# Optimization experiments

Hardware: AMD Instinct MI355X
Metric: run time of the kernel (lower is better)

The kernel has to match this reference:

```python
import jax, jax.numpy as jnp
import numpy as np

N = 64
K_CHEB = 5
EPS = 1e-5

# db4 decomposition filters (scaling_filter.mat Lo_D / Hi_D, length 8)
_LO = np.array([-0.010597401784997278, 0.032883011666982945, 0.030841381835986965,
                -0.18703481171888114, -0.02798376941698385, 0.6308807679295904,
                0.7148465705525415, 0.23037781330885523], dtype=np.float32)
_HI = np.array([-0.23037781330885523, 0.7148465705525415, -0.6308807679295904,
                -0.02798376941698385, 0.18703481171888114, 0.030841381835986965,
                0.032883011666982945, -0.010597401784997278], dtype=np.float32)
# torch stores np.flip(filters) and Conv2d does cross-correlation -> use flipped taps here too
_KERN = np.stack([_LO[::-1], _HI[::-1]])[:, None, None, :].copy()  # [2,1,1,8]


def _wavelet_step(x):
    # x: [B, C, 1, W]; circular pad 3 each side, depthwise len-8 conv, stride 2
    p = 3  # filter_length // 2 - 1
    xp = jnp.concatenate([x[..., -p:], x, x[..., :p]], axis=-1)
    b, c, h, wp = xp.shape
    out = jax.lax.conv_general_dilated(
        xp.reshape(b * c, 1, h, wp), jnp.asarray(_KERN), (1, 2), 'VALID',
        dimension_numbers=('NCHW', 'OIHW', 'NCHW'))
    out = out.reshape(b, c, 2, h, -1)
    return out[:, :, 0], out[:, :, 1]  # (approx, detail)


def _cbam(x, fc1, fc2, sa_w):
    # x: [B, 657, 1, 64]; channel attention then spatial attention
    def mlp(v):  # v: [B, C, 1, 1]
        h = jax.nn.relu(jnp.einsum('oc,bchw->bohw', fc1, v))
        return jnp.einsum('oc,bchw->bohw', fc2, h)
    avg = x.mean(axis=(2, 3), keepdims=True)
    mx = x.max(axis=(2, 3), keepdims=True)
    x = x * jax.nn.sigmoid(mlp(avg) + mlp(mx))
    s = jnp.concatenate([x.mean(axis=1, keepdims=True), x.max(axis=1, keepdims=True)], axis=1)
    sa = jax.nn.sigmoid(jax.lax.conv_general_dilated(
        s, sa_w, (1, 1), ((3, 3), (3, 3)), dimension_numbers=('NCHW', 'OIHW', 'NCHW')))
    return x * sa


def _global_edge_weight(w_tril, mask):
    xs, ys = np.tril_indices(N)
    E = jnp.zeros((N, N), w_tril.dtype).at[xs, ys].set(w_tril)
    E = E + E.T - jnp.diag(jnp.diag(E))
    return (E * mask).reshape(-1)


def _norm_adj(edges, w):
    # PyG NewSGConv.norm: add remaining self-loops (fill=1), deg from |w|, sym normalize
    row, col = edges[0], edges[1]
    has_self = jnp.zeros((N,), w.dtype).at[row].add(jnp.where(row == col, 1.0, 0.0)) > 0
    w_self = jnp.where(has_self, 0.0, 1.0).astype(w.dtype)
    deg = jnp.zeros((N,), w.dtype).at[row].add(jnp.abs(w)) + w_self
    dsafe = jnp.where(deg > 0, deg, 1.0)
    dinv = jnp.where(deg > 0, jax.lax.rsqrt(dsafe), 0.0)
    norm = dinv[row] * w * dinv[col]
    A = jnp.zeros((N, N), w.dtype).at[col, row].add(norm)  # out[i] = sum_j A[i,j] x[j]
    return A + jnp.diag(dinv * w_self * dinv)


def _gcn_block(x, A, W, b, g, be):
    # x: [B, N, C_in]; K-hop SGConv propagation, linear, train-mode batchnorm over (B, N)
    for _ in range(K_CHEB):
        x = jnp.einsum('ij,bjc->bic', A, x)
    x = x @ W.T + b
    mean = x.mean(axis=(0, 1))
    var = x.var(axis=(0, 1))
    return (x - mean) * jax.lax.rsqrt(var + EPS) * g + be


def _classify(x, W1, b1, g, be, W2, b2):
    out = x.reshape(x.shape[0], -1) @ W1.T + b1
    out = (out - out.mean(0)) * jax.lax.rsqrt(out.var(0) + EPS) * g + be
    return jax.nn.log_softmax(out @ W2.T + b2, axis=1)


def _forward(x, local_graph_weight, global_mask, ca_fc1, ca_fc2, sa_conv, edge_weight_tril,
             ld_W, ld_b, ld_g, ld_be, ld1_W, ld1_b, ld1_g, ld1_be,
             d_W, d_b, d_g, d_be, d1_W, d1_b, d1_g, d1_be,
             cls_W1, cls_b1, cls_g, cls_be, cls_W2, cls_b2, edges):
    xc = jnp.transpose(x, (0, 3, 2, 1))        # [B, 657, 1, 64]
    xc = _cbam(xc, ca_fc1, ca_fc2, sa_conv)
    xh = jnp.transpose(xc, (0, 3, 2, 1))       # [B, 64, 1, 657]
    # fi = floor(log2(200)) = 7 -> 4 decomposition levels: 657->328->164->82->41
    out1, _gamma = _wavelet_step(xh)
    out2, _beta = _wavelet_step(out1)
    out3, _alpha = _wavelet_step(out2)
    delta, _theta = _wavelet_step(out3)        # [B, 64, 1, 41]
    delta = delta[:, :, 0, :]                  # squeeze -> [B, 64, 41]
    gw = _global_edge_weight(edge_weight_tril, global_mask)
    A_loc = _norm_adj(edges, local_graph_weight)
    A_glb = _norm_adj(edges, gw)
    lf = _gcn_block(delta, A_loc, ld_W, ld_b, ld_g, ld_be)
    lf = _gcn_block(lf, A_loc, ld1_W, ld1_b, ld1_g, ld1_be)
    gf = _gcn_block(delta, A_glb, d_W, d_b, d_g, d_be)
    gf = _gcn_block(gf, A_glb, d1_W, d1_b, d1_g, d1_be)
    feat = jnp.concatenate([lf.mean(-1, keepdims=True), gf.mean(-1, keepdims=True)], axis=2)  # [B,64,2]
    return _classify(feat, cls_W1, cls_b1, cls_g, cls_be, cls_W2, cls_b2)


def setup_inputs() -> dict:
    key = jax.random.key(0)
    ks = iter(jax.random.split(key, 16))
    B = 512
    f32 = jnp.float32
    def rn(shape, s=0.05):
        return jax.random.normal(next(ks), shape, f32) * s
    ii = jnp.arange(N, dtype=jnp.int32)
    edges = jnp.stack([jnp.repeat(ii, N), jnp.tile(ii, N)])  # full 64x64 mesh (incl. self loops)
    return dict(
        x=jax.random.normal(next(ks), (B, N, 1, 657), f32),
        local_graph_weight=jax.random.uniform(next(ks), (N * N,), f32),
        global_mask=jnp.ones((N, N), f32),
        ca_fc1=rn((82, 657)),
        ca_fc2=rn((657, 82)),
        sa_conv=rn((1, 2, 7, 7), 0.1),
        edge_weight_tril=jax.random.uniform(next(ks), (N * (N + 1) // 2,), f32),
        ld_W=rn((16, 41)), ld_b=jnp.zeros(16, f32), ld_g=jnp.ones(16, f32), ld_be=jnp.zeros(16, f32),
        ld1_W=rn((4, 16)), ld1_b=jnp.zeros(4, f32), ld1_g=jnp.ones(4, f32), ld1_be=jnp.zeros(4, f32),
        d_W=rn((16, 41)), d_b=jnp.zeros(16, f32), d_g=jnp.ones(16, f32), d_be=jnp.zeros(16, f32),
        d1_W=rn((4, 16)), d1_b=jnp.zeros(4, f32), d1_g=jnp.ones(4, f32), d1_be=jnp.zeros(4, f32),
        cls_W1=rn((32, 128)), cls_b1=jnp.zeros(32, f32), cls_g=jnp.ones(32, f32), cls_be=jnp.zeros(32, f32),
        cls_W2=rn((2, 32)), cls_b2=jnp.zeros(2, f32),
        edges=edges,
    )


def reference(x, local_graph_weight, global_mask, ca_fc1, ca_fc2, sa_conv, edge_weight_tril,
              ld_W, ld_b, ld_g, ld_be, ld1_W, ld1_b, ld1_g, ld1_be,
              d_W, d_b, d_g, d_be, d1_W, d1_b, d1_g, d1_be,
              cls_W1, cls_b1, cls_g, cls_be, cls_W2, cls_b2, edges):
    return _forward(x, local_graph_weight, global_mask, ca_fc1, ca_fc2, sa_conv, edge_weight_tril,
                    ld_W, ld_b, ld_g, ld_be, ld1_W, ld1_b, ld1_g, ld1_be,
                    d_W, d_b, d_g, d_be, d1_W, d1_b, d1_g, d1_be,
                    cls_W1, cls_b1, cls_g, cls_be, cls_W2, cls_b2, edges)
```

## Files before the change

kernel.cpp:

```cpp
#include <hip/hip_runtime.h>
#include <math.h>

#define NB 512
#define NN 64
#define TL 657
#define LV1 328
#define LV2 164
#define LV3 82
#define LV4 41
#define HID 82
#define ST 66

#define WS_M      0
#define WS_ACC    32768
#define WS_SMEAN  36864
#define WS_SMAX   167936
#define WS_CATT   3373568
#define WS_Y1     682496
#define WS_DELTA  4876800
#define WS_Y2     4876800
#define WS_OUT1   5925376

#define ACC_Y1 0
#define ACC_Y2 64
#define ACC_O1 80

__device__ __forceinline__ float sigmoidf_(float v){ return 1.0f/(1.0f+expf(-v)); }

__device__ __forceinline__ void wav_level(float* __restrict__ dst, const float* __restrict__ src,
                                          int outL, int inL, int lane){
  const float DLO[8] = {0.23037781330885523f, 0.7148465705525415f, 0.6308807679295904f,
                        -0.02798376941698385f, -0.18703481171888114f, 0.030841381835986965f,
                        0.032883011666982945f, -0.010597401784997278f};
  for (int k=lane; k<outL; k+=64){
    int i0 = 2*k - 3;
    float a = 0.f;
    #pragma unroll
    for (int j=0;j<8;j++){
      int idx = i0 + j;
      idx = (idx < 0) ? idx + inL : ((idx >= inL) ? idx - inL : idx);
      a += src[idx]*DLO[j];
    }
    dst[k] = a;
  }
}

__device__ __forceinline__ void mm16(float* __restrict__ D, int dstride,
                                     const float* __restrict__ A, const float* __restrict__ Bm){
  int tid = threadIdx.x;
  int wv = tid >> 6, lane = tid & 63;
  int i0 = wv*4;
  float a4[4] = {0.f,0.f,0.f,0.f};
  #pragma unroll
  for (int kc=0; kc<4; kc++){
    float bb[16];
    #pragma unroll
    for (int j=0;j<16;j++) bb[j] = Bm[(kc*16+j)*ST + lane];
    #pragma unroll
    for (int i=0;i<4;i++){
      const float2* ar = (const float2*)&A[(i0+i)*ST + kc*16];
      float s0=0.f, s1=0.f;
      #pragma unroll
      for (int j2=0;j2<8;j2++){
        float2 v = ar[j2];
        s0 += v.x*bb[2*j2]; s1 += v.y*bb[2*j2+1];
      }
      a4[i] += s0+s1;
    }
  }
  #pragma unroll
  for (int i=0;i<4;i++) D[(i0+i)*dstride + lane] = a4[i];
}

__global__ __launch_bounds__(1024) void k_front(
    const float* __restrict__ x,
    const float* __restrict__ lgw, const float* __restrict__ gmask,
    const float* __restrict__ tril, const int* __restrict__ edges,
    const float* __restrict__ fc1, const float* __restrict__ fc2,
    float* __restrict__ catt_g,
    float* __restrict__ Mout, double* __restrict__ acc)
{
  __shared__ float smem[3*NN*ST];
  __shared__ float deg[64], hs[64], dinv[64], wself[64];
  int tid = threadIdx.x;
  int bid = blockIdx.x;
  int wv = tid>>6, lane = tid&63;
  int b = bid;

  if (bid < 2){
    float* Wbuf = smem;
    float* Amat = smem + NN*ST;
    float* P1   = smem + 2*NN*ST;
    int g = bid;
    if (g==0 && tid<512) acc[tid]=0.0;
    for (int e=tid;e<4096;e+=1024){
      float w;
      if (g==0) w = lgw[e];
      else {
        int i=e>>6, j=e&63;
        int aa = (i>j)? i:j, bb = (i>j)? j:i;
        w = tril[aa*(aa+1)/2 + bb] * gmask[e];
      }
      Wbuf[e] = w;
    }
    for (int i=tid;i<NN*ST;i+=1024) Amat[i] = 0.f;
    if (tid<64){ deg[tid]=0.f; hs[tid]=0.f; }
    __syncthreads();
    {
      int e0 = tid*4;
      int runr = edges[e0];
      float runv = 0.f;
      #pragma unroll
      for (int i=0;i<4;i++){
        int e = e0+i;
        int r = edges[e];
        int c = edges[4096+e];
        float w = Wbuf[e];
        if (r != runr){ atomicAdd(&deg[runr], runv); runr = r; runv = 0.f; }
        runv += fabsf(w);
        if (r == c) hs[r] = 1.f;
      }
      atomicAdd(&deg[runr], runv);
    }
    __syncthreads();
    if (tid<64){
      float w_ = (hs[tid] > 0.f) ? 0.f : 1.f;
      float d = deg[tid] + w_;
      dinv[tid] = (d > 0.f) ? rsqrtf(d) : 0.f;
      wself[tid] = w_;
    }
    __syncthreads();
    for (int e=tid;e<4096;e+=1024){
      int r = edges[e], c = edges[4096+e];
      float nm = dinv[r]*Wbuf[e]*dinv[c];
      atomicAdd(&Amat[c*ST+r], nm);
    }
    __syncthreads();
    if (tid<64) Amat[tid*ST+tid] += dinv[tid]*wself[tid]*dinv[tid];
    __syncthreads();
    mm16(P1,   ST, Amat, Amat); __syncthreads();
    mm16(Wbuf, ST, P1,   P1);   __syncthreads();
    mm16(&Mout[g*4096], 64, Wbuf, Amat);
    __syncthreads();
  }

  {
    float s[11], m[11];
    #pragma unroll
    for (int i=0;i<11;i++){ s[i]=0.f; m[i]=-INFINITY; }
    const float* xb = x + (size_t)b*NN*TL;
    for (int r=0;r<4;r++){
      const float* row = xb + (size_t)(wv*4 + r)*TL;
      #pragma unroll
      for (int i=0;i<11;i++){
        int t = lane + 64*i;
        if (t < TL){
          float v = row[t];
          s[i] += v; m[i] = fmaxf(m[i], v);
        }
      }
    }
    for (int step=8; step>=1; step>>=1){
      if (wv >= step && wv < 2*step){
        float* bs = smem + (wv-step)*1328;
        #pragma unroll
        for (int i=0;i<11;i++){
          int t = lane + 64*i;
          if (t<TL){ bs[t] = s[i]; bs[664+t] = m[i]; }
        }
      }
      __syncthreads();
      if (wv < step){
        float* bs = smem + wv*1328;
        #pragma unroll
        for (int i=0;i<11;i++){
          int t = lane + 64*i;
          if (t<TL){ s[i] += bs[t]; m[i] = fmaxf(m[i], bs[664+t]); }
        }
      }
      __syncthreads();
    }
    float* cs = smem;
    float* cm = smem + 664;
    float* h  = smem + 1400;
    if (wv==0){
      #pragma unroll
      for (int i=0;i<11;i++){
        int t = lane + 64*i;
        if (t<TL){ cs[t] = s[i]; cm[t] = m[i]; }
      }
    }
    __syncthreads();
    for (int o=wv; o<HID; o+=16){
      const float* fr = fc1 + (size_t)o*TL;
      float a = 0.f, bm = 0.f;
      #pragma unroll
      for (int i=0;i<11;i++){
        int c = lane + 64*i;
        if (c < TL){
          float f = fr[c];
          a += f*cs[c]; bm += f*cm[c];
        }
      }
      #pragma unroll
      for (int off=32;off;off>>=1){
        a  += __shfl_xor(a,off);
        bm += __shfl_xor(bm,off);
      }
      if (lane==0)
        h[o] = fmaxf(a*(1.0f/64.0f),0.f) + fmaxf(bm,0.f);
    }
    __syncthreads();
    if (tid < TL){
      const float2* fr = (const float2*)(fc2 + (size_t)tid*HID);
      float a0=0.f, a1=0.f;
      #pragma unroll
      for (int u2=0;u2<41;u2++){
        float2 v = fr[u2];
        a0 += v.x*h[2*u2]; a1 += v.y*h[2*u2+1];
      }
      catt_g[(size_t)b*TL + tid] = sigmoidf_(a0+a1);
    }
  }
}

__global__ __launch_bounds__(256) void k_wav(
    const float* __restrict__ x, const float* __restrict__ catt_g,
    float* __restrict__ delta, float* __restrict__ smean, float* __restrict__ smax)
{
  __shared__ float catt[TL];
  __shared__ float yb[4][TL];
  __shared__ float o1b[4][LV1];
  __shared__ float o2b[4][LV2];
  __shared__ float o3b[4][LV3];
  int tid = threadIdx.x, b = blockIdx.x;
  for (int i=tid;i<TL;i+=256) catt[i] = catt_g[(size_t)b*TL + i];
  __syncthreads();
  int wv = tid>>6, lane = tid&63;
  int n = blockIdx.y*4 + wv;
  float* y  = yb[wv];
  float* p1 = o1b[wv];
  float* p2 = o2b[wv];
  float* p3 = o3b[wv];
  const float DLO[8] = {0.23037781330885523f, 0.7148465705525415f, 0.6308807679295904f,
                        -0.02798376941698385f, -0.18703481171888114f, 0.030841381835986965f,
                        0.032883011666982945f, -0.010597401784997278f};
  const float* row = x + ((size_t)b*NN + n)*TL;
  float ls = 0.f, lm = -INFINITY;
  #pragma unroll
  for (int i=0;i<11;i++){
    int t = lane + 64*i;
    if (t < TL){
      float v = row[t]*catt[t];
      y[t] = v; ls += v; lm = fmaxf(lm,v);
    }
  }
  #pragma unroll
  for (int off=32;off;off>>=1){
    ls += __shfl_xor(ls,off);
    lm = fmaxf(lm, __shfl_xor(lm,off));
  }
  if (lane==0){ smean[b*NN+n] = ls*(1.0f/657.0f); smax[b*NN+n] = lm; }
  wav_level(p1, y,  LV1, TL,  lane);
  wav_level(p2, p1, LV2, LV1, lane);
  wav_level(p3, p2, LV3, LV2, lane);
  if (lane < LV4){
    int i0 = 2*lane - 3;
    float a = 0.f;
    #pragma unroll
    for (int j=0;j<8;j++){
      int idx = i0 + j;
      idx = (idx < 0) ? idx + LV3 : ((idx >= LV3) ? idx - LV3 : idx);
      a += p3[idx]*DLO[j];
    }
    delta[((size_t)b*NN + n)*LV4 + lane] = a;
  }
}

__global__ __launch_bounds__(256) void k_gcn1(
  const float* __restrict__ delta, const float* __restrict__ Mmat,
  const float* __restrict__ smean, const float* __restrict__ smax,
  const float* __restrict__ saw,
  const float* __restrict__ ldW, const float* __restrict__ ldb,
  const float* __restrict__ dW, const float* __restrict__ db2,
  float* __restrict__ Y1, double* __restrict__ acc)
{
  __shared__ float Dl[NN*LV4];
  __shared__ float Tt[NN*16];
  __shared__ float Mm[4096];
  __shared__ float Wl[16*LV4];
  __shared__ float satt[NN];
  __shared__ double red[256];
  int tid=threadIdx.x, b=blockIdx.x;
  if (tid < NN){
    float a = 0.f;
    #pragma unroll
    for (int kw=0;kw<7;kw++){
      int w = tid + kw - 3;
      if (0<=w && w<NN) a += smean[b*NN+w]*saw[21+kw] + smax[b*NN+w]*saw[70+kw];
    }
    satt[tid] = sigmoidf_(a);
  }
  __syncthreads();
  const float* ds = delta + (size_t)b*NN*LV4;
  for (int i=tid;i<NN*LV4;i+=256) Dl[i] = ds[i]*satt[i/LV4];
  for (int g=0; g<2; g++){
    const float* Ws = g ? dW : ldW;
    const float* bs = g ? db2 : ldb;
    for (int i=tid;i<16*LV4;i+=256) Wl[i]=Ws[i];
    for (int i=tid;i<4096;i+=256) Mm[i]=Mmat[g*4096+i];
    __syncthreads();
    for (int e=tid;e<NN*16;e+=256){
      int n=e>>4, o=e&15;
      const float* dr=&Dl[n*LV4];
      const float* wr=&Wl[o*LV4];
      float a=0.f;
      #pragma unroll 8
      for (int c=0;c<LV4;c++) a += dr[c]*wr[c];
      Tt[e]=a;
    }
    __syncthreads();
    float bias = bs[tid&15];
    float ps=0.f, pq=0.f;
    for (int m=0;m<4;m++){
      int e=tid+256*m;
      int n=e>>4, o=e&15;
      float a=bias;
      #pragma unroll 8
      for (int k=0;k<64;k++) a += Mm[n*64+k]*Tt[k*16+o];
      Y1[((size_t)b*NN+n)*32 + g*16 + o] = a;
      ps += a; pq += a*a;
    }
    red[tid]=(double)ps;
    __syncthreads();
    if (tid<16){ double t=0; for (int r=tid;r<256;r+=16) t+=red[r]; atomicAdd(&acc[ACC_Y1+g*32+tid], t); }
    __syncthreads();
    red[tid]=(double)pq;
    __syncthreads();
    if (tid<16){ double t=0; for (int r=tid;r<256;r+=16) t+=red[r]; atomicAdd(&acc[ACC_Y1+g*32+16+tid], t); }
    __syncthreads();
  }
}

__global__ __launch_bounds__(256) void k_gcn2(
  const float* __restrict__ Y1, const float* __restrict__ Mmat,
  const float* __restrict__ ldg, const float* __restrict__ ldbe,
  const float* __restrict__ dg, const float* __restrict__ dbe,
  const float* __restrict__ ld1W, const float* __restrict__ ld1b,
  const float* __restrict__ d1W, const float* __restrict__ d1b,
  float* __restrict__ Y2, double* __restrict__ acc)
{
  __shared__ float Yl[NN*32];
  __shared__ float T2[NN*8];
  __shared__ float Mm[2*4096];
  __shared__ float scl[32], sht[32];
  __shared__ double red[256];
  int tid=threadIdx.x, b=blockIdx.x;
  const float* ys = Y1 + (size_t)b*NN*32;
  for (int i=tid;i<NN*32;i+=256) Yl[i]=ys[i];
  for (int i=tid;i<8192;i+=256) Mm[i]=Mmat[i];
  if (tid<32){
    int g=tid>>4, o=tid&15;
    double s=acc[ACC_Y1+g*32+o], q=acc[ACC_Y1+g*32+16+o];
    double mean=s/32768.0;
    double var=q/32768.0 - mean*mean;
    float gam = g? dg[o] : ldg[o];
    float bet = g? dbe[o] : ldbe[o];
    float sc = gam * rsqrtf((float)var + 1e-5f);
    scl[tid]=sc; sht[tid]=bet - (float)mean*sc;
  }
  __syncthreads();
  for (int i=tid;i<NN*32;i+=256){ int c=i&31; Yl[i]=Yl[i]*scl[c]+sht[c]; }
  __syncthreads();
  for (int e=tid;e<NN*8;e+=256){
    int n=e>>3, c=e&7, g=c>>2, p=c&3;
    const float* w = (g? d1W : ld1W) + p*16;
    const float* yr = &Yl[n*32 + g*16];
    float a=0.f;
    #pragma unroll
    for (int o=0;o<16;o++) a += yr[o]*w[o];
    T2[e]=a;
  }
  __syncthreads();
  float ps=0.f,pq=0.f;
  for (int m=0;m<2;m++){
    int e=tid+256*m;
    int n=e>>3, c=e&7, g=c>>2;
    float a = g? d1b[c&3] : ld1b[c&3];
    const float* mr=&Mm[g*4096+n*64];
    #pragma unroll 8
    for (int k=0;k<64;k++) a += mr[k]*T2[k*8+c];
    Y2[((size_t)b*NN+n)*8 + c] = a;
    ps+=a; pq+=a*a;
  }
  red[tid]=(double)ps; __syncthreads();
  if (tid<8){ double t=0; for (int r=tid;r<256;r+=8) t+=red[r]; atomicAdd(&acc[ACC_Y2 + (tid>>2)*8 + (tid&3)], t); }
  __syncthreads();
  red[tid]=(double)pq; __syncthreads();
  if (tid<8){ double t=0; for (int r=tid;r<256;r+=8) t+=red[r]; atomicAdd(&acc[ACC_Y2 + (tid>>2)*8 + 4 + (tid&3)], t); }
}

__global__ __launch_bounds__(64) void k_featcls(
  const float* __restrict__ Y2,
  const float* __restrict__ ld1g, const float* __restrict__ ld1be,
  const float* __restrict__ d1g, const float* __restrict__ d1be,
  const float* __restrict__ W1, const float* __restrict__ b1,
  float* __restrict__ out1, double* __restrict__ acc)
{
  __shared__ float f[128];
  __shared__ float scl[8], sht[8];
  int tid=threadIdx.x, b=blockIdx.x;
  if (tid<8){
    int g=tid>>2, p=tid&3;
    double s=acc[ACC_Y2+g*8+p], q=acc[ACC_Y2+g*8+4+p];
    double mean=s/32768.0;
    double var=q/32768.0-mean*mean;
    float gam = g? d1g[p]:ld1g[p];
    float bet = g? d1be[p]:ld1be[p];
    float sc = gam*rsqrtf((float)var+1e-5f);
    scl[tid]=sc; sht[tid]=bet-(float)mean*sc;
  }
  __syncthreads();
  {
    const float* yr = Y2 + ((size_t)b*NN+tid)*8;
    float lf=0.f, gf=0.f;
    #pragma unroll
    for (int p=0;p<4;p++){
      lf += yr[p]*scl[p]+sht[p];
      gf += yr[4+p]*scl[4+p]+sht[4+p];
    }
    f[2*tid]   = lf*0.25f;
    f[2*tid+1] = gf*0.25f;
  }
  __syncthreads();
  if (tid<32){
    const float* w = W1 + tid*128;
    float a = b1[tid];
    #pragma unroll 4
    for (int m=0;m<128;m++) a += w[m]*f[m];
    out1[b*32+tid]=a;
    atomicAdd(&acc[ACC_O1+tid], (double)a);
    atomicAdd(&acc[ACC_O1+32+tid], (double)(a*a));
  }
}

__global__ __launch_bounds__(64) void k_cls2(
  const float* __restrict__ out1,
  const float* __restrict__ cg, const float* __restrict__ cbe,
  const float* __restrict__ W2, const float* __restrict__ b2,
  const double* __restrict__ acc, float* __restrict__ out)
{
  __shared__ float v[32];
  __shared__ float z[2];
  int tid=threadIdx.x, b=blockIdx.x;
  if (tid<32){
    double s=acc[ACC_O1+tid], q=acc[ACC_O1+32+tid];
    double mean=s/512.0;
    double var=q/512.0-mean*mean;
    float sc=cg[tid]*rsqrtf((float)var+1e-5f);
    float sh=cbe[tid]-(float)mean*sc;
    v[tid]=out1[b*32+tid]*sc+sh;
  }
  __syncthreads();
  if (tid<2){
    const float* w=W2+tid*32;
    float a=b2[tid];
    #pragma unroll
    for (int j=0;j<32;j++) a += w[j]*v[j];
    z[tid]=a;
  }
  __syncthreads();
  if (tid<2){
    float m=fmaxf(z[0],z[1]);
    float l=m+logf(expf(z[0]-m)+expf(z[1]-m));
    out[b*2+tid]=z[tid]-l;
  }
}

extern "C" void kernel_launch(void* const* d_in, const int* in_sizes, int n_in,
                              void* d_out, int out_size, void* d_ws, size_t ws_size,
                              hipStream_t stream) {
  (void)in_sizes; (void)n_in; (void)out_size; (void)ws_size;
  const float* x     = (const float*)d_in[0];
  const float* lgw   = (const float*)d_in[1];
  const float* gmask = (const float*)d_in[2];
  const float* fc1   = (const float*)d_in[3];
  const float* fc2   = (const float*)d_in[4];
  const float* saw   = (const float*)d_in[5];
  const float* tril  = (const float*)d_in[6];
  const float* ldW   = (const float*)d_in[7];
  const float* ldb   = (const float*)d_in[8];
  const float* ldg   = (const float*)d_in[9];
  const float* ldbe  = (const float*)d_in[10];
  const float* ld1W  = (const float*)d_in[11];
  const float* ld1b  = (const float*)d_in[12];
  const float* ld1g  = (const float*)d_in[13];
  const float* ld1be = (const float*)d_in[14];
  const float* dW    = (const float*)d_in[15];
  const float* db2   = (const float*)d_in[16];
  const float* dg    = (const float*)d_in[17];
  const float* dbe   = (const float*)d_in[18];
  const float* d1W   = (const float*)d_in[19];
  const float* d1b   = (const float*)d_in[20];
  const float* d1g   = (const float*)d_in[21];
  const float* d1be  = (const float*)d_in[22];
  const float* cW1   = (const float*)d_in[23];
  const float* cb1   = (const float*)d_in[24];
  const float* cgam  = (const float*)d_in[25];
  const float* cbet  = (const float*)d_in[26];
  const float* cW2   = (const float*)d_in[27];
  const float* cb2   = (const float*)d_in[28];
  const int*   edges = (const int*)d_in[29];

  char* ws = (char*)d_ws;
  float*  M     = (float*)(ws + WS_M);
  double* acc   = (double*)(ws + WS_ACC);
  float*  smean = (float*)(ws + WS_SMEAN);
  float*  smax  = (float*)(ws + WS_SMAX);
  float*  catt  = (float*)(ws + WS_CATT);
  float*  Y1    = (float*)(ws + WS_Y1);
  float*  delta = (float*)(ws + WS_DELTA);
  float*  Y2    = (float*)(ws + WS_Y2);
  float*  out1  = (float*)(ws + WS_OUT1);
  float*  out   = (float*)d_out;

  k_front<<<NB, 1024, 0, stream>>>(x, lgw, gmask, tril, edges, fc1, fc2,
                                   catt, M, acc);
  k_wav<<<dim3(NB, 16), 256, 0, stream>>>(x, catt, delta, smean, smax);
  k_gcn1<<<NB, 256, 0, stream>>>(delta, M, smean, smax, saw, ldW, ldb, dW, db2, Y1, acc);
  k_gcn2<<<NB, 256, 0, stream>>>(Y1, M, ldg, ldbe, dg, dbe, ld1W, ld1b, d1W, d1b, Y2, acc);
  k_featcls<<<NB, 64, 0, stream>>>(Y2, ld1g, ld1be, d1g, d1be, cW1, cb1, out1, acc);
  k_cls2<<<NB, 64, 0, stream>>>(out1, cgam, cbet, cW2, cb2, acc, out);
}
```

Before: 160.0 us.

## Split graph power computation across dedicated blocks and halve front block size

The A^5 graph propagation matrices were previously computed serially inside two of the per-batch blocks, which delayed those blocks. Now 32 dedicated blocks each compute four rows of A^5 by repeated row-times-matrix products (each block rebuilds the normalized adjacency redundantly), and the batch blocks no longer carry that work. The front kernel also drops from 1024 to 512 threads per block, with each wave handling more rows, which may improve occupancy and reduce the cost of the reduction tree. The trade-offs are redundant adjacency construction in every graph block and less parallelism within each batch block.

```diff
diff --git a/kernel.cpp b/kernel.cpp
--- a/kernel.cpp
+++ b/kernel.cpp
@@ -10,6 +10,7 @@
 #define LV4 41
 #define HID 82
 #define ST 66
+#define NGB 32
 
 #define WS_M      0
 #define WS_ACC    32768
@@ -45,34 +46,7 @@
   }
 }
 
-__device__ __forceinline__ void mm16(float* __restrict__ D, int dstride,
-                                     const float* __restrict__ A, const float* __restrict__ Bm){
-  int tid = threadIdx.x;
-  int wv = tid >> 6, lane = tid & 63;
-  int i0 = wv*4;
-  float a4[4] = {0.f,0.f,0.f,0.f};
-  #pragma unroll
-  for (int kc=0; kc<4; kc++){
-    float bb[16];
-    #pragma unroll
-    for (int j=0;j<16;j++) bb[j] = Bm[(kc*16+j)*ST + lane];
-    #pragma unroll
-    for (int i=0;i<4;i++){
-      const float2* ar = (const float2*)&A[(i0+i)*ST + kc*16];
-      float s0=0.f, s1=0.f;
-      #pragma unroll
-      for (int j2=0;j2<8;j2++){
-        float2 v = ar[j2];
-        s0 += v.x*bb[2*j2]; s1 += v.y*bb[2*j2+1];
-      }
-      a4[i] += s0+s1;
-    }
-  }
-  #pragma unroll
-  for (int i=0;i<4;i++) D[(i0+i)*dstride + lane] = a4[i];
-}
-
-__global__ __launch_bounds__(1024) void k_front(
+__global__ __launch_bounds__(512) void k_front(
     const float* __restrict__ x,
     const float* __restrict__ lgw, const float* __restrict__ gmask,
     const float* __restrict__ tril, const int* __restrict__ edges,
@@ -85,15 +59,16 @@
   int tid = threadIdx.x;
   int bid = blockIdx.x;
   int wv = tid>>6, lane = tid&63;
-  int b = bid;
-
-  if (bid < 2){
+
+  if (bid < NGB){
+    int g  = bid >> 4;
+    int s4 = (bid & 15) * 4;
     float* Wbuf = smem;
     float* Amat = smem + NN*ST;
-    float* P1   = smem + 2*NN*ST;
-    int g = bid;
-    if (g==0 && tid<512) acc[tid]=0.0;
-    for (int e=tid;e<4096;e+=1024){
+    float* Rc   = smem + 2*NN*ST;
+    float* Rn   = Rc + 4*ST;
+    if (bid==0 && tid<512) acc[tid]=0.0;
+    for (int e=tid;e<4096;e+=512){
       float w;
       if (g==0) w = lgw[e];
       else {
@@ -103,15 +78,15 @@
       }
       Wbuf[e] = w;
     }
-    for (int i=tid;i<NN*ST;i+=1024) Amat[i] = 0.f;
+    for (int i=tid;i<NN*ST;i+=512) Amat[i] = 0.f;
     if (tid<64){ deg[tid]=0.f; hs[tid]=0.f; }
     __syncthreads();
     {
-      int e0 = tid*4;
+      int e0 = tid*8;
       int runr = edges[e0];
       float runv = 0.f;
       #pragma unroll
-      for (int i=0;i<4;i++){
+      for (int i=0;i<8;i++){
         int e = e0+i;
         int r = edges[e];
         int c = edges[4096+e];
@@ -130,7 +105,7 @@
       wself[tid] = w_;
     }
     __syncthreads();
-    for (int e=tid;e<4096;e+=1024){
+    for (int e=tid;e<4096;e+=512){
       int r = edges[e], c = edges[4096+e];
       float nm = dinv[r]*Wbuf[e]*dinv[c];
       atomicAdd(&Amat[c*ST+r], nm);
@@ -138,19 +113,42 @@
     __syncthreads();
     if (tid<64) Amat[tid*ST+tid] += dinv[tid]*wself[tid]*dinv[tid];
     __syncthreads();
-    mm16(P1,   ST, Amat, Amat); __syncthreads();
-    mm16(Wbuf, ST, P1,   P1);   __syncthreads();
-    mm16(&Mout[g*4096], 64, Wbuf, Amat);
-    __syncthreads();
-  }
-
+    if (tid < 256){
+      int r = tid>>6, c = tid&63;
+      Rc[r*ST+c] = Amat[(s4+r)*ST+c];
+    }
+    __syncthreads();
+    #pragma unroll
+    for (int it=0; it<4; it++){
+      if (tid < 256){
+        int r = tid>>6, c = tid&63;
+        const float* rr = &Rc[r*ST];
+        float a0=0.f, a1=0.f;
+        #pragma unroll 8
+        for (int k=0;k<64;k+=2){
+          a0 += rr[k]  *Amat[k*ST+c];
+          a1 += rr[k+1]*Amat[(k+1)*ST+c];
+        }
+        Rn[r*ST+c] = a0+a1;
+      }
+      __syncthreads();
+      float* t = Rc; Rc = Rn; Rn = t;
+    }
+    if (tid < 256){
+      int r = tid>>6, c = tid&63;
+      Mout[g*4096 + (s4+r)*64 + c] = Rc[r*ST+c];
+    }
+    return;
+  }
+
+  int b = bid - NGB;
   {
     float s[11], m[11];
     #pragma unroll
     for (int i=0;i<11;i++){ s[i]=0.f; m[i]=-INFINITY; }
     const float* xb = x + (size_t)b*NN*TL;
-    for (int r=0;r<4;r++){
-      const float* row = xb + (size_t)(wv*4 + r)*TL;
+    for (int r=0;r<8;r++){
+      const float* row = xb + (size_t)(wv*8 + r)*TL;
       #pragma unroll
       for (int i=0;i<11;i++){
         int t = lane + 64*i;
@@ -160,7 +158,7 @@
         }
       }
     }
-    for (int step=8; step>=1; step>>=1){
+    for (int step=4; step>=1; step>>=1){
       if (wv >= step && wv < 2*step){
         float* bs = smem + (wv-step)*1328;
         #pragma unroll
@@ -191,7 +189,7 @@
       }
     }
     __syncthreads();
-    for (int o=wv; o<HID; o+=16){
+    for (int o=wv; o<HID; o+=8){
       const float* fr = fc1 + (size_t)o*TL;
       float a = 0.f, bm = 0.f;
       #pragma unroll
@@ -211,15 +209,15 @@
         h[o] = fmaxf(a*(1.0f/64.0f),0.f) + fmaxf(bm,0.f);
     }
     __syncthreads();
-    if (tid < TL){
-      const float2* fr = (const float2*)(fc2 + (size_t)tid*HID);
+    for (int c=tid; c<TL; c+=512){
+      const float2* fr = (const float2*)(fc2 + (size_t)c*HID);
       float a0=0.f, a1=0.f;
       #pragma unroll
       for (int u2=0;u2<41;u2++){
         float2 v = fr[u2];
         a0 += v.x*h[2*u2]; a1 += v.y*h[2*u2+1];
       }
-      catt_g[(size_t)b*TL + tid] = sigmoidf_(a0+a1);
+      catt_g[(size_t)b*TL + c] = sigmoidf_(a0+a1);
     }
   }
 }
@@ -524,8 +522,8 @@
   float*  out1  = (float*)(ws + WS_OUT1);
   float*  out   = (float*)d_out;
 
-  k_front<<<NB, 1024, 0, stream>>>(x, lgw, gmask, tril, edges, fc1, fc2,
-                                   catt, M, acc);
+  k_front<<<NB + NGB, 512, 0, stream>>>(x, lgw, gmask, tril, edges, fc1, fc2,
+                                        catt, M, acc);
   k_wav<<<dim3(NB, 16), 256, 0, stream>>>(x, catt, delta, smean, smax);
   k_gcn1<<<NB, 256, 0, stream>>>(delta, M, smean, smax, saw, ldW, ldb, dW, db2, Y1, acc);
   k_gcn2<<<NB, 256, 0, stream>>>(Y1, M, ldg, ldbe, dg, dbe, ld1W, ld1b, d1W, d1b, Y2, acc);
```

Result: slower. 168.4 us (+5.3%).
